# Optimization experiments

Hardware: AMD Instinct MI355X
Metric: run time of the kernel (lower is better)

## Reference

```python
import jax, jax.numpy as jnp
import numpy as np

N = 10000   # nodes
E = 320000  # edges
D = 3000    # input genes
H1, H2 = 1024, 128
F1, F2, F3, F4 = 256, 512, 1024, 2048
BN_EPS = 1e-5

def setup_inputs() -> dict:
    key = jax.random.key(0)
    ks = jax.random.split(key, 30)
    rn = lambda k, s, sc=0.05: jax.random.normal(k, s, dtype=jnp.float32) * sc
    inp = {}
    inp["x"] = jax.random.normal(ks[0], (N, D), dtype=jnp.float32)
    inp["edge_w"] = jax.random.uniform(ks[1], (E,), dtype=jnp.float32)
    inp["W1"] = rn(ks[2], (D, H1))
    inp["W2"] = rn(ks[3], (H1, H2))
    inp["W3"] = rn(ks[4], (H1, H2))
    dims = [(H2, F1), (F1, F2), (F2, F3), (F3, F4), (F4, D)]
    for i, (di, do) in enumerate(dims, start=1):
        inp[f"fc{i}_w"] = rn(ks[4 + i], (di, do))
        inp[f"fc{i}_b"] = jnp.zeros((do,), jnp.float32)
        if i <= 4:
            inp[f"bn{i}_g"] = jnp.ones((do,), jnp.float32)
            inp[f"bn{i}_b"] = jnp.zeros((do,), jnp.float32)
    inp["edge_src"] = jax.random.randint(ks[20], (E,), 0, N)
    inp["edge_dst"] = jax.random.randint(ks[21], (E,), 0, N)
    return inp

def reference(x, edge_w, W1, W2, W3,
              fc1_w, fc1_b, bn1_g, bn1_b,
              fc2_w, fc2_b, bn2_g, bn2_b,
              fc3_w, fc3_b, bn3_g, bn3_b,
              fc4_w, fc4_b, bn4_g, bn4_b,
              fc5_w, fc5_b, edge_src, edge_dst):
    # sparse adjacency matmul: out[dst] += w * h[src]
    def spmm(h):
        return jax.ops.segment_sum(h[edge_src] * edge_w[:, None], edge_dst, num_segments=N)
    # GCN encoder: GraphConvolution = act(adj @ (x @ W)) (dropout inactive in eval)
    h1 = jax.nn.relu(spmm(x @ W1))
    mu = spmm(h1 @ W2)
    logvar = spmm(h1 @ W3)
    z = mu  # eval-mode reparameterize returns mu
    # inner-product adjacency decoder (act = identity)
    adj_rec = z @ z.T
    # FC stack: Linear -> BatchNorm(eval, running mean=0, var=1) -> ReLU
    inv = 1.0 / jnp.sqrt(jnp.float32(1.0 + BN_EPS))
    def fc(h, w, b, g, be):
        return jax.nn.relu((h @ w + b) * inv * g + be)
    o = fc(z, fc1_w, fc1_b, bn1_g, bn1_b)
    o = fc(o, fc2_w, fc2_b, bn2_g, bn2_b)
    o = fc(o, fc3_w, fc3_b, bn3_g, bn3_b)
    o = fc(o, fc4_w, fc4_b, bn4_g, bn4_b)
    x_rec = o @ fc5_w + fc5_b  # fc5: no batchnorm, identity act
    return (adj_rec, mu, logvar, z, x_rec)
```

## Files before the change

kernel.cpp:

```cpp
#include <hip/hip_runtime.h>
#include <stdint.h>

typedef unsigned short ushort_t;
typedef __attribute__((ext_vector_type(8))) short short8;
typedef __attribute__((ext_vector_type(4))) float f32x4;

#define N_NODES 10000
#define MP      10240
#define E_EDGES 320000
#define D_IN    3000
#define K1P     3008
#define H1      1024
#define H2      128

static __device__ __forceinline__ float b2f(ushort_t u) {
  union { uint32_t u; float f; } x; x.u = ((uint32_t)u) << 16; return x.f;
}
static __device__ __forceinline__ ushort_t f2b(float f) {
  union { float f; uint32_t u; } x; x.f = f;
  uint32_t r = x.u + 0x7FFF + ((x.u >> 16) & 1);
  return (ushort_t)(r >> 16);
}

static __device__ __forceinline__ void gload16(const void* g, void* l) {
  __builtin_amdgcn_global_load_lds(
      (const __attribute__((address_space(1))) uint32_t*)g,
      (__attribute__((address_space(3))) uint32_t*)l, 16, 0, 0);
}

__global__ void zero_k(int* p, int n) {
  int i = blockIdx.x * 256 + threadIdx.x;
  if (i < n) p[i] = 0;
}
__global__ void count_k(const int* __restrict__ ed, int* __restrict__ cnt) {
  int e = blockIdx.x * 256 + threadIdx.x;
  if (e < E_EDGES) atomicAdd(&cnt[ed[e]], 1);
}
__global__ void scan_k(const int* __restrict__ cnt, int* __restrict__ rs, int* __restrict__ cur) {
  __shared__ int sums[256];
  int t = threadIdx.x;
  const int per = 40;
  int base = t * per;
  int s = 0;
  for (int i = 0; i < per; i++) { int idx = base + i; if (idx < N_NODES) s += cnt[idx]; }
  sums[t] = s;
  __syncthreads();
  if (t == 0) { int run = 0; for (int i = 0; i < 256; i++) { int v = sums[i]; sums[i] = run; run += v; } }
  __syncthreads();
  int run = sums[t];
  for (int i = 0; i < per; i++) {
    int idx = base + i;
    if (idx < N_NODES) { rs[idx] = run; cur[idx] = run; run += cnt[idx]; }
  }
  if (t == 255) rs[N_NODES] = run;
}
__global__ void fill_k(const int* __restrict__ es, const int* __restrict__ ed,
                       const float* __restrict__ ew,
                       int* __restrict__ cur, int* __restrict__ psrc, float* __restrict__ pw) {
  int e = blockIdx.x * 256 + threadIdx.x;
  if (e >= E_EDGES) return;
  int d = ed[e];
  int pos = atomicAdd(&cur[d], 1);
  psrc[pos] = es[e];
  pw[pos] = ew[e];
}

__global__ void conv_x_k(const float* __restrict__ x, ushort_t* __restrict__ xb) {
  int g = blockIdx.x * 256 + threadIdx.x;
  int row = g / 376;
  int c8 = (g % 376) * 8;
  float v[8];
  if (row < N_NODES && c8 < 3000) {
    const float4 f0 = *(const float4*)(x + (size_t)row * 3000 + c8);
    const float4 f1 = *(const float4*)(x + (size_t)row * 3000 + c8 + 4);
    v[0]=f0.x; v[1]=f0.y; v[2]=f0.z; v[3]=f0.w;
    v[4]=f1.x; v[5]=f1.y; v[6]=f1.z; v[7]=f1.w;
  } else {
#pragma unroll
    for (int i = 0; i < 8; i++) v[i] = 0.f;
  }
  uint32_t o0 = (uint32_t)f2b(v[0]) | ((uint32_t)f2b(v[1]) << 16);
  uint32_t o1 = (uint32_t)f2b(v[2]) | ((uint32_t)f2b(v[3]) << 16);
  uint32_t o2 = (uint32_t)f2b(v[4]) | ((uint32_t)f2b(v[5]) << 16);
  uint32_t o3 = (uint32_t)f2b(v[6]) | ((uint32_t)f2b(v[7]) << 16);
  uint4 ov; ov.x=o0; ov.y=o1; ov.z=o2; ov.w=o3;
  *(uint4*)&xb[(size_t)row * K1P + c8] = ov;
}

struct Seg { const float* src; ushort_t* dst; int K, Nn, Kp, Np, tilesN, blk0; };
struct SegPack { Seg s[8]; };
__global__ void conv_w_all_k(SegPack P) {
  __shared__ float tile[32][33];
  int b = blockIdx.x;
  int si = 0;
#pragma unroll
  for (int i = 1; i < 8; ++i) if (b >= P.s[i].blk0) si = i;
  Seg sg = P.s[si];
  int rel = b - sg.blk0;
  int tk = rel / sg.tilesN, tn = rel % sg.tilesN;
  int tx = threadIdx.x & 31, ty0 = threadIdx.x >> 5;
#pragma unroll
  for (int i = 0; i < 4; ++i) {
    int ty = ty0 + i * 8;
    int k = tk * 32 + ty, n = tn * 32 + tx;
    tile[ty][tx] = (k < sg.K && n < sg.Nn) ? sg.src[(size_t)k * sg.Nn + n] : 0.f;
  }
  __syncthreads();
#pragma unroll
  for (int i = 0; i < 4; ++i) {
    int ty = ty0 + i * 8;
    int n = tn * 32 + ty, k = tk * 32 + tx;
    sg.dst[(size_t)n * sg.Kp + k] = f2b(tile[tx][ty]);
  }
}

template<int EPI>
__global__ __launch_bounds__(256)
void gemm_bt(const ushort_t* __restrict__ A, const ushort_t* __restrict__ BT, int K,
             void* __restrict__ outp, int ldOut, int realM, int realN,
             const float* __restrict__ bias, const float* __restrict__ bng,
             const float* __restrict__ bnb)
{
  __shared__ ushort_t lA[128 * 32];
  __shared__ ushort_t lB[128 * 32];
  const int tid  = threadIdx.x;
  const int row0 = blockIdx.x * 128;
  const int col0 = blockIdx.y * 128;
  const int lane = tid & 63;
  const int wave = tid >> 6;
  const int wr = (wave >> 1) * 64, wc = (wave & 1) * 64;
  const int fr = lane & 15, fq = lane >> 4;

  f32x4 acc[4][4] = {};

  const int rA = tid >> 2;
  const int cA = (tid & 3) * 8;
  const ushort_t* Ab = A  + (size_t)(row0 + rA) * K + cA;
  const ushort_t* Bb = BT + (size_t)(col0 + rA) * K + cA;
  ushort_t* lA0 = &lA[tid * 8];
  ushort_t* lA1 = &lA[2048 + tid * 8];
  ushort_t* lB0 = &lB[tid * 8];
  ushort_t* lB1 = &lB[2048 + tid * 8];
  const size_t rstep = (size_t)64 * K;

  for (int k0 = 0; k0 < K; k0 += 32) {
    gload16(Ab + k0,         lA0);
    gload16(Ab + rstep + k0, lA1);
    gload16(Bb + k0,         lB0);
    gload16(Bb + rstep + k0, lB1);
    __syncthreads();
    short8 af[4], bv[4];
#pragma unroll
    for (int m = 0; m < 4; m++) af[m] = *(const short8*)&lA[(wr + m * 16 + fr) * 32 + fq * 8];
#pragma unroll
    for (int n = 0; n < 4; n++) bv[n] = *(const short8*)&lB[(wc + n * 16 + fr) * 32 + fq * 8];
#pragma unroll
    for (int m = 0; m < 4; m++)
#pragma unroll
      for (int n = 0; n < 4; n++)
        acc[m][n] = __builtin_amdgcn_mfma_f32_16x16x32_bf16(af[m], bv[n], acc[m][n], 0, 0, 0);
    __syncthreads();
  }

  const float inv = 0.9999950000374997f;
#pragma unroll
  for (int n = 0; n < 4; n++) {
    int col = col0 + wc + n * 16 + fr;
    float s = 0.f, t = 0.f, bb = 0.f;
    if (EPI == 1) { s = inv * bng[col]; t = bias[col] * s + bnb[col]; }
    if (EPI == 2) { bb = (col < realN) ? bias[col] : 0.f; }
#pragma unroll
    for (int m = 0; m < 4; m++) {
      int rowb = row0 + wr + m * 16 + fq * 4;
#pragma unroll
      for (int r = 0; r < 4; r++) {
        int row = rowb + r;
        float v = acc[m][n][r];
        if (EPI == 0) {
          ((ushort_t*)outp)[(size_t)row * ldOut + col] = f2b(v);
        } else if (EPI == 1) {
          v = fmaxf(v * s + t, 0.f);
          ((ushort_t*)outp)[(size_t)row * ldOut + col] = f2b(v);
        } else if (EPI == 2) {
          if (row < realM && col < realN)
            ((float*)outp)[(size_t)row * ldOut + col] = v + bb;
        } else {
          if (row < realM && col < realN)
            ((float*)outp)[(size_t)row * ldOut + col] = v;
        }
      }
    }
  }
}

template<int WM, int WN, int MR, int NR, int EPI>
__global__ __launch_bounds__(512, 2)
void gemm_p(const ushort_t* __restrict__ A, const ushort_t* __restrict__ BT, int K,
            void* __restrict__ outp, int ldOut, int realM, int realN,
            const float* __restrict__ bias, const float* __restrict__ bng,
            const float* __restrict__ bnb)
{
  constexpr int BM  = WM * MR * 16;
  constexpr int BN  = WN * NR * 16;
  constexpr int ALD = (BM * 4) / 512;
  constexpr int BLD = (BN * 4) / 512;
  __shared__ ushort_t lA[2 * BM * 32];
  __shared__ ushort_t lB[2 * BN * 32];

  const int tid  = threadIdx.x;
  const int wave = tid >> 6;
  const int wm = wave / WN, wn = wave % WN;
  const int fr = tid & 15, fq = (tid >> 4) & 3;
  const int row0 = blockIdx.x * BM;
  const int col0 = blockIdx.y * BN;

  f32x4 acc[MR][NR] = {};

  auto stA = [&](int p, int kt, int r) {
    int c = r * 512 + tid;
    int row = c >> 2, slot = c & 3;
    int ss = slot ^ ((row >> 1) & 3);
    gload16(A + (size_t)(row0 + row) * K + kt * 32 + ss * 8,
            &lA[p * (BM * 32) + c * 8]);
  };
  auto stB = [&](int p, int kt, int r) {
    int c = r * 512 + tid;
    int row = c >> 2, slot = c & 3;
    int ss = slot ^ ((row >> 1) & 3);
    gload16(BT + (size_t)(col0 + row) * K + kt * 32 + ss * 8,
            &lB[p * (BN * 32) + c * 8]);
  };

  const int NT = K >> 5;
#pragma unroll
  for (int r = 0; r < ALD; ++r) stA(0, 0, r);
#pragma unroll
  for (int r = 0; r < BLD; ++r) stB(0, 0, r);

  for (int t = 0; t < NT; ++t) {
    const int p = t & 1, q = p ^ 1;
    const int tn = (t + 1 < NT) ? t + 1 : NT - 1;
#pragma unroll
    for (int r = 0; r < ALD; ++r) stA(q, tn, r);
    asm volatile("s_waitcnt vmcnt(2)" ::: "memory");
    asm volatile("" ::: "memory");
    __builtin_amdgcn_s_barrier();
    asm volatile("" ::: "memory");

    short8 bf[NR];
#pragma unroll
    for (int n = 0; n < NR; ++n) {
      int rb = wn * (NR * 16) + n * 16 + fr;
      bf[n] = *(const short8*)&lB[p * (BN * 32) + rb * 32 + ((fq ^ ((rb >> 1) & 3)) * 8)];
    }
    {
      short8 af[MR / 2];
#pragma unroll
      for (int m = 0; m < MR / 2; ++m) {
        int ra = wm * (MR * 16) + m * 16 + fr;
        af[m] = *(const short8*)&lA[p * (BM * 32) + ra * 32 + ((fq ^ ((ra >> 1) & 3)) * 8)];
      }
      __builtin_amdgcn_s_setprio(1);
#pragma unroll
      for (int m = 0; m < MR / 2; ++m)
#pragma unroll
        for (int n = 0; n < NR; ++n)
          acc[m][n] = __builtin_amdgcn_mfma_f32_16x16x32_bf16(af[m], bf[n], acc[m][n], 0, 0, 0);
      __builtin_amdgcn_s_setprio(0);
    }
#pragma unroll
    for (int r = 0; r < BLD; ++r) stB(q, tn, r);
    asm volatile("" ::: "memory");
    __builtin_amdgcn_s_barrier();
    asm volatile("" ::: "memory");
    {
      short8 af[MR - MR / 2];
#pragma unroll
      for (int m = 0; m < MR - MR / 2; ++m) {
        int ra = wm * (MR * 16) + (m + MR / 2) * 16 + fr;
        af[m] = *(const short8*)&lA[p * (BM * 32) + ra * 32 + ((fq ^ ((ra >> 1) & 3)) * 8)];
      }
      __builtin_amdgcn_s_setprio(1);
#pragma unroll
      for (int m = 0; m < MR - MR / 2; ++m)
#pragma unroll
        for (int n = 0; n < NR; ++n)
          acc[m + MR / 2][n] = __builtin_amdgcn_mfma_f32_16x16x32_bf16(af[m], bf[n], acc[m + MR / 2][n], 0, 0, 0);
      __builtin_amdgcn_s_setprio(0);
    }
    asm volatile("" ::: "memory");
    __builtin_amdgcn_s_barrier();
    asm volatile("" ::: "memory");
  }

  const float inv = 0.9999950000374997f;
#pragma unroll
  for (int n = 0; n < NR; ++n) {
    int col = col0 + wn * (NR * 16) + n * 16 + fr;
    float s = 0.f, t = 0.f, bb = 0.f;
    if (EPI == 1) { s = inv * bng[col]; t = bias[col] * s + bnb[col]; }
    if (EPI == 2) { bb = (col < realN) ? bias[col] : 0.f; }
#pragma unroll
    for (int m = 0; m < MR; ++m) {
      int rowb = row0 + wm * (MR * 16) + m * 16 + fq * 4;
#pragma unroll
      for (int r = 0; r < 4; ++r) {
        int row = rowb + r;
        float v = acc[m][n][r];
        if (EPI == 0) {
          ((ushort_t*)outp)[(size_t)row * ldOut + col] = f2b(v);
        } else if (EPI == 1) {
          v = fmaxf(v * s + t, 0.f);
          ((ushort_t*)outp)[(size_t)row * ldOut + col] = f2b(v);
        } else if (EPI == 2) {
          if (row < realM && col < realN)
            ((float*)outp)[(size_t)row * ldOut + col] = v + bb;
        } else {
          if (row < realM && col < realN)
            ((float*)outp)[(size_t)row * ldOut + col] = v;
        }
      }
    }
  }
}

__global__ void spmm1_k(const ushort_t* __restrict__ h, ushort_t* __restrict__ o,
                        const int* __restrict__ rs, const int* __restrict__ psrc,
                        const float* __restrict__ pw) {
  int dst = blockIdx.x;
  int t = threadIdx.x;
  float a0 = 0.f, a1 = 0.f, a2 = 0.f, a3 = 0.f;
  if (dst < N_NODES) {
    int s0 = rs[dst], e0 = rs[dst + 1];
    for (int i = s0; i < e0; ++i) {
      float wv = pw[i];
      uint2 v = *(const uint2*)&h[(size_t)psrc[i] * H1 + t * 4];
      a0 += wv * b2f((ushort_t)(v.x & 0xffff));
      a1 += wv * b2f((ushort_t)(v.x >> 16));
      a2 += wv * b2f((ushort_t)(v.y & 0xffff));
      a3 += wv * b2f((ushort_t)(v.y >> 16));
    }
  }
  uint2 ov;
  ov.x = (uint32_t)f2b(fmaxf(a0, 0.f)) | ((uint32_t)f2b(fmaxf(a1, 0.f)) << 16);
  ov.y = (uint32_t)f2b(fmaxf(a2, 0.f)) | ((uint32_t)f2b(fmaxf(a3, 0.f)) << 16);
  *(uint2*)&o[(size_t)dst * H1 + t * 4] = ov;
}
__global__ void spmm2_k(const ushort_t* __restrict__ pre, float* __restrict__ mu,
                        float* __restrict__ lv, float* __restrict__ zf,
                        ushort_t* __restrict__ zb,
                        const int* __restrict__ rs, const int* __restrict__ psrc,
                        const float* __restrict__ pw) {
  int dst = blockIdx.x;
  int t = threadIdx.x;
  float acc = 0.f;
  if (dst < N_NODES) {
    int s = rs[dst], e = rs[dst + 1];
    for (int i = s; i < e; i++)
      acc += pw[i] * b2f(pre[(size_t)psrc[i] * 256 + t]);
  }
  if (t < 128) {
    zb[(size_t)dst * 128 + t] = f2b(acc);
    if (dst < N_NODES) {
      mu[(size_t)dst * 128 + t] = acc;
      zf[(size_t)dst * 128 + t] = acc;
    }
  } else if (dst < N_NODES) {
    lv[(size_t)dst * 128 + (t - 128)] = acc;
  }
}

extern "C" void kernel_launch(void* const* d_in, const int* in_sizes, int n_in,
                              void* d_out, int out_size, void* d_ws, size_t ws_size,
                              hipStream_t stream) {
  (void)in_sizes; (void)n_in; (void)out_size; (void)ws_size;
  const float* x  = (const float*)d_in[0];
  const float* ew = (const float*)d_in[1];
  const float* W1 = (const float*)d_in[2];
  const float* W2 = (const float*)d_in[3];
  const float* W3 = (const float*)d_in[4];
  const float* fc_w[5] = {(const float*)d_in[5], (const float*)d_in[9],  (const float*)d_in[13], (const float*)d_in[17], (const float*)d_in[21]};
  const float* fc_b[5] = {(const float*)d_in[6], (const float*)d_in[10], (const float*)d_in[14], (const float*)d_in[18], (const float*)d_in[22]};
  const float* bn_g[4] = {(const float*)d_in[7], (const float*)d_in[11], (const float*)d_in[15], (const float*)d_in[19]};
  const float* bn_b[4] = {(const float*)d_in[8], (const float*)d_in[12], (const float*)d_in[16], (const float*)d_in[20]};
  const int* esrc = (const int*)d_in[23];
  const int* edst = (const int*)d_in[24];
  float* out = (float*)d_out;

  float* out_adj = out;
  float* out_mu  = out + (size_t)100000000;
  float* out_lv  = out + (size_t)101280000;
  float* out_z   = out + (size_t)102560000;
  float* out_xr  = out + (size_t)103840000;

  char* w = (char*)d_ws;
  size_t off = 0;
  auto alloc = [&](size_t bytes) { size_t o = off; off = (off + bytes + 255) & ~(size_t)255; return o; };
  int*      cnt  = (int*)(w + alloc(4 * N_NODES));
  int*      rs   = (int*)(w + alloc(4 * (N_NODES + 1)));
  int*      cur  = (int*)(w + alloc(4 * N_NODES));
  int*      psrc = (int*)(w + alloc(4 * E_EDGES));
  float*    pw   = (float*)(w + alloc(4 * E_EDGES));
  ushort_t* w1T  = (ushort_t*)(w + alloc((size_t)2 * 1024 * K1P));
  ushort_t* w23T = (ushort_t*)(w + alloc((size_t)2 * 256 * 1024));
  ushort_t* f1T  = (ushort_t*)(w + alloc((size_t)2 * 256 * 128));
  ushort_t* f2T  = (ushort_t*)(w + alloc((size_t)2 * 512 * 256));
  ushort_t* f3T  = (ushort_t*)(w + alloc((size_t)2 * 1024 * 512));
  ushort_t* f4T  = (ushort_t*)(w + alloc((size_t)2 * 2048 * 1024));
  ushort_t* f5T  = (ushort_t*)(w + alloc((size_t)2 * 3072 * 2048));
  ushort_t* xb   = (ushort_t*)(w + alloc((size_t)2 * MP * K1P));
  ushort_t* xw1b = (ushort_t*)(w + alloc((size_t)2 * MP * H1));
  ushort_t* h1b  = (ushort_t*)(w + alloc((size_t)2 * MP * H1));
  ushort_t* preb = (ushort_t*)(w + alloc((size_t)2 * MP * 256));
  ushort_t* zb   = (ushort_t*)(w + alloc((size_t)2 * MP * 128));
  ushort_t* act1 = xw1b;
  ushort_t* act2 = xb;
  ushort_t* act3 = h1b;
  ushort_t* act4 = xb;

  zero_k<<<(N_NODES + 255) / 256, 256, 0, stream>>>(cnt, N_NODES);
  count_k<<<(E_EDGES + 255) / 256, 256, 0, stream>>>(edst, cnt);
  scan_k<<<1, 256, 0, stream>>>(cnt, rs, cur);
  fill_k<<<(E_EDGES + 255) / 256, 256, 0, stream>>>(esrc, edst, ew, cur, psrc, pw);

  conv_x_k<<<(MP * 376) / 256, 256, 0, stream>>>(x, xb);
  {
    SegPack P;
    int b0 = 0;
    auto mk = [&](const float* s, ushort_t* d, int K, int Nn, int Kp, int Np) {
      Seg sg; sg.src = s; sg.dst = d; sg.K = K; sg.Nn = Nn; sg.Kp = Kp; sg.Np = Np;
      sg.tilesN = Np / 32; sg.blk0 = b0;
      b0 += (Kp / 32) * (Np / 32);
      return sg;
    };
    P.s[0] = mk(W1,      w1T,                       D_IN, 1024, K1P,  1024);
    P.s[1] = mk(W2,      w23T,                      1024, 128,  1024, 128);
    P.s[2] = mk(W3,      w23T + (size_t)128 * 1024, 1024, 128,  1024, 128);
    P.s[3] = mk(fc_w[0], f1T,                       128,  256,  128,  256);
    P.s[4] = mk(fc_w[1], f2T,                       256,  512,  256,  512);
    P.s[5] = mk(fc_w[2], f3T,                       512,  1024, 512,  1024);
    P.s[6] = mk(fc_w[3], f4T,                       1024, 2048, 1024, 2048);
    P.s[7] = mk(fc_w[4], f5T,                       2048, 3000, 2048, 3072);
    conv_w_all_k<<<b0, 256, 0, stream>>>(P);
  }

  dim3 blk2(256), blk5(512);
  gemm_p<4,2,4,4,0><<<dim3(MP / 256, 1024 / 128), blk5, 0, stream>>>(xb, w1T, K1P, xw1b, 1024, MP, 1024, nullptr, nullptr, nullptr);
  spmm1_k<<<dim3(MP), blk2, 0, stream>>>(xw1b, h1b, rs, psrc, pw);
  gemm_bt<0><<<dim3(MP / 128, 2), blk2, 0, stream>>>(h1b, w23T, 1024, preb, 256, MP, 256, nullptr, nullptr, nullptr);
  spmm2_k<<<dim3(MP), blk2, 0, stream>>>(preb, out_mu, out_lv, out_z, zb, rs, psrc, pw);
  gemm_bt<3><<<dim3(MP / 128, MP / 128), blk2, 0, stream>>>(zb, zb, 128, out_adj, 10000, N_NODES, N_NODES, nullptr, nullptr, nullptr);
  gemm_bt<1><<<dim3(MP / 128, 2), blk2, 0, stream>>>(zb, f1T, 128, act1, 256, MP, 256, fc_b[0], bn_g[0], bn_b[0]);
  gemm_p<4,2,4,4,1><<<dim3(MP / 256, 512 / 128),  blk5, 0, stream>>>(act1, f2T, 256,  act2, 512,  MP, 512,  fc_b[1], bn_g[1], bn_b[1]);
  gemm_p<4,2,4,4,1><<<dim3(MP / 256, 1024 / 128), blk5, 0, stream>>>(act2, f3T, 512,  act3, 1024, MP, 1024, fc_b[2], bn_g[2], bn_b[2]);
  gemm_p<2,4,8,4,1><<<dim3(MP / 256, 2048 / 256), blk5, 0, stream>>>(act3, f4T, 1024, act4, 2048, MP, 2048, fc_b[3], bn_g[3], bn_b[3]);
  gemm_p<2,4,8,4,2><<<dim3(MP / 256, 3072 / 256), blk5, 0, stream>>>(act4, f5T, 2048, out_xr, 3000, N_NODES, 3000, fc_b[4], nullptr, nullptr);
}
```

Baseline: 874.4 us.

## Triple-buffer LDS in gemm_p and route decoder and fc4 through it

```diff
diff --git a/kernel.cpp b/kernel.cpp
--- a/kernel.cpp
+++ b/kernel.cpp
@@ -193,19 +193,21 @@
   }
 }
 
-template<int WM, int WN, int MR, int NR, int EPI>
-__global__ __launch_bounds__(512, 2)
+template<int WM, int WN, int MR, int NR, int EPI, int MINW>
+__global__ __launch_bounds__(WM * WN * 64, MINW)
 void gemm_p(const ushort_t* __restrict__ A, const ushort_t* __restrict__ BT, int K,
             void* __restrict__ outp, int ldOut, int realM, int realN,
             const float* __restrict__ bias, const float* __restrict__ bng,
             const float* __restrict__ bnb)
 {
+  constexpr int T   = WM * WN * 64;
   constexpr int BM  = WM * MR * 16;
   constexpr int BN  = WN * NR * 16;
-  constexpr int ALD = (BM * 4) / 512;
-  constexpr int BLD = (BN * 4) / 512;
-  __shared__ ushort_t lA[2 * BM * 32];
-  __shared__ ushort_t lB[2 * BN * 32];
+  constexpr int ALD = (BM * 32) / (T * 8);
+  constexpr int BLD = (BN * 32) / (T * 8);
+  constexpr int NVM = 2 * (ALD + BLD);
+  __shared__ ushort_t lA[3 * BM * 32];
+  __shared__ ushort_t lB[3 * BN * 32];
 
   const int tid  = threadIdx.x;
   const int wave = tid >> 6;
@@ -217,14 +219,14 @@
   f32x4 acc[MR][NR] = {};
 
   auto stA = [&](int p, int kt, int r) {
-    int c = r * 512 + tid;
+    int c = r * T + tid;
     int row = c >> 2, slot = c & 3;
     int ss = slot ^ ((row >> 1) & 3);
     gload16(A + (size_t)(row0 + row) * K + kt * 32 + ss * 8,
             &lA[p * (BM * 32) + c * 8]);
   };
   auto stB = [&](int p, int kt, int r) {
-    int c = r * 512 + tid;
+    int c = r * T + tid;
     int row = c >> 2, slot = c & 3;
     int ss = slot ^ ((row >> 1) & 3);
     gload16(BT + (size_t)(col0 + row) * K + kt * 32 + ss * 8,
@@ -236,13 +238,21 @@
   for (int r = 0; r < ALD; ++r) stA(0, 0, r);
 #pragma unroll
   for (int r = 0; r < BLD; ++r) stB(0, 0, r);
+#pragma unroll
+  for (int r = 0; r < ALD; ++r) stA(1, 1, r);
+#pragma unroll
+  for (int r = 0; r < BLD; ++r) stB(1, 1, r);
 
   for (int t = 0; t < NT; ++t) {
-    const int p = t & 1, q = p ^ 1;
-    const int tn = (t + 1 < NT) ? t + 1 : NT - 1;
-#pragma unroll
-    for (int r = 0; r < ALD; ++r) stA(q, tn, r);
-    asm volatile("s_waitcnt vmcnt(2)" ::: "memory");
+    const int p = t % 3;
+    const int s = (t + 2) % 3;
+    const int ts = (t + 2 < NT) ? t + 2 : NT - 1;
+#pragma unroll
+    for (int r = 0; r < ALD; ++r) stA(s, ts, r);
+#pragma unroll
+    for (int r = 0; r < BLD; ++r) stB(s, ts, r);
+    if constexpr (NVM == 6) asm volatile("s_waitcnt vmcnt(6)" ::: "memory");
+    else                    asm volatile("s_waitcnt vmcnt(8)" ::: "memory");
     asm volatile("" ::: "memory");
     __builtin_amdgcn_s_barrier();
     asm volatile("" ::: "memory");
@@ -268,11 +278,6 @@
           acc[m][n] = __builtin_amdgcn_mfma_f32_16x16x32_bf16(af[m], bf[n], acc[m][n], 0, 0, 0);
       __builtin_amdgcn_s_setprio(0);
     }
-#pragma unroll
-    for (int r = 0; r < BLD; ++r) stB(q, tn, r);
-    asm volatile("" ::: "memory");
-    __builtin_amdgcn_s_barrier();
-    asm volatile("" ::: "memory");
     {
       short8 af[MR - MR / 2];
 #pragma unroll
@@ -445,14 +450,14 @@
   }
 
   dim3 blk2(256), blk5(512);
-  gemm_p<4,2,4,4,0><<<dim3(MP / 256, 1024 / 128), blk5, 0, stream>>>(xb, w1T, K1P, xw1b, 1024, MP, 1024, nullptr, nullptr, nullptr);
+  gemm_p<4,2,4,4,0,4><<<dim3(MP / 256, 1024 / 128), blk5, 0, stream>>>(xb, w1T, K1P, xw1b, 1024, MP, 1024, nullptr, nullptr, nullptr);
   spmm1_k<<<dim3(MP), blk2, 0, stream>>>(xw1b, h1b, rs, psrc, pw);
   gemm_bt<0><<<dim3(MP / 128, 2), blk2, 0, stream>>>(h1b, w23T, 1024, preb, 256, MP, 256, nullptr, nullptr, nullptr);
   spmm2_k<<<dim3(MP), blk2, 0, stream>>>(preb, out_mu, out_lv, out_z, zb, rs, psrc, pw);
-  gemm_bt<3><<<dim3(MP / 128, MP / 128), blk2, 0, stream>>>(zb, zb, 128, out_adj, 10000, N_NODES, N_NODES, nullptr, nullptr, nullptr);
+  gemm_p<2,4,8,4,3,2><<<dim3(MP / 256, MP / 256), blk5, 0, stream>>>(zb, zb, 128, out_adj, 10000, N_NODES, N_NODES, nullptr, nullptr, nullptr);
   gemm_bt<1><<<dim3(MP / 128, 2), blk2, 0, stream>>>(zb, f1T, 128, act1, 256, MP, 256, fc_b[0], bn_g[0], bn_b[0]);
-  gemm_p<4,2,4,4,1><<<dim3(MP / 256, 512 / 128),  blk5, 0, stream>>>(act1, f2T, 256,  act2, 512,  MP, 512,  fc_b[1], bn_g[1], bn_b[1]);
-  gemm_p<4,2,4,4,1><<<dim3(MP / 256, 1024 / 128), blk5, 0, stream>>>(act2, f3T, 512,  act3, 1024, MP, 1024, fc_b[2], bn_g[2], bn_b[2]);
-  gemm_p<2,4,8,4,1><<<dim3(MP / 256, 2048 / 256), blk5, 0, stream>>>(act3, f4T, 1024, act4, 2048, MP, 2048, fc_b[3], bn_g[3], bn_b[3]);
-  gemm_p<2,4,8,4,2><<<dim3(MP / 256, 3072 / 256), blk5, 0, stream>>>(act4, f5T, 2048, out_xr, 3000, N_NODES, 3000, fc_b[4], nullptr, nullptr);
-}
+  gemm_p<4,2,4,4,1,4><<<dim3(MP / 256, 512 / 128),  blk5, 0, stream>>>(act1, f2T, 256,  act2, 512,  MP, 512,  fc_b[1], bn_g[1], bn_b[1]);
+  gemm_p<4,2,4,4,1,4><<<dim3(MP / 256, 1024 / 128), blk5, 0, stream>>>(act2, f3T, 512,  act3, 1024, MP, 1024, fc_b[2], bn_g[2], bn_b[2]);
+  gemm_p<4,2,4,4,1,4><<<dim3(MP / 256, 2048 / 128), blk5, 0, stream>>>(act3, f4T, 1024, act4, 2048, MP, 2048, fc_b[3], bn_g[3], bn_b[3]);
+  gemm_p<2,4,8,4,2,2><<<dim3(MP / 256, 3072 / 256), blk5, 0, stream>>>(act4, f5T, 2048, out_xr, 3000, N_NODES, 3000, fc_b[4], nullptr, nullptr);
+}
```

Result: no change. 858.7 us (-1.8%).
